# Kernel tuning notes

Hardware: AMD Instinct MI355X
Metric: run time of the kernel (lower is better)

## Reference

```python
import jax, jax.numpy as jnp
import numpy as np

B = 262144  # batch of joint configurations (original module processes one at a time)


def setup_inputs() -> dict:
    key = jax.random.key(0)
    k = jax.random.split(key, 7)
    joints = jax.random.normal(k[0], (B, 7), dtype=jnp.float32)
    # fk_params rows: (alpha, a, d, theta_offset) per joint
    fk_params = jax.random.normal(k[1], (7, 4), dtype=jnp.float32) * 0.5
    # nn.Linear(7,15), nn.Linear(15,15), nn.Linear(15,7): y = x @ W.T + b
    W1 = jax.random.normal(k[2], (15, 7), dtype=jnp.float32) * 0.3
    b1 = jax.random.normal(k[3], (15,), dtype=jnp.float32) * 0.1
    W2 = jax.random.normal(k[4], (15, 15), dtype=jnp.float32) * 0.3
    b2 = jax.random.normal(k[5], (15,), dtype=jnp.float32) * 0.1
    W3 = jax.random.normal(k[6], (7, 15), dtype=jnp.float32) * 0.3
    b3 = jnp.zeros((7,), dtype=jnp.float32)
    return {"joints": joints, "fk_params": fk_params,
            "W1": W1, "b1": b1, "W2": W2, "b2": b2, "W3": W3, "b3": b3}


def reference(joints, fk_params, W1, b1, W2, b2, W3, b3):
    # 7-15-15-7 tanh MLP correction
    h = jnp.tanh(joints @ W1.T + b1)
    h = jnp.tanh(h @ W2.T + b2)
    correction = jnp.tanh(h @ W3.T + b3)
    theta = joints + correction                         # [B,7]

    alpha = fk_params[:, 0]                             # [7]
    a = fk_params[:, 1]
    d = fk_params[:, 2]
    offset = fk_params[:, 3]

    th = theta + offset                                 # [B,7]
    ct, st = jnp.cos(th), jnp.sin(th)                   # [B,7]
    ca, sa = jnp.cos(alpha), jnp.sin(alpha)             # [7]
    z = jnp.zeros_like(ct)
    o = jnp.ones_like(ct)

    # DH transform per (batch, joint): [B,7,4,4]
    row0 = jnp.stack([ct,      -st,       z,       a * o      ], axis=-1)
    row1 = jnp.stack([st * ca,  ct * ca, -sa * o, -d * sa * o ], axis=-1)
    row2 = jnp.stack([st * sa,  ct * sa,  ca * o,  ca * d * o ], axis=-1)
    row3 = jnp.stack([z,        z,        z,       o          ], axis=-1)
    M = jnp.stack([row0, row1, row2, row3], axis=-2)    # [B,7,4,4]

    # serial chain multiply over the 7 joints (fixed, small loop)
    ee = M[:, 0]
    for j in range(1, 7):
        ee = ee @ M[:, j]

    # wrist_transform[:-1, -1] -> translation part
    return ee[:, :3, 3]                                 # [B,3]
```

## Files before the change

kernel.cpp:

```cpp
#include <hip/hip_runtime.h>
#include <math.h>

#define BLK 256

__device__ __forceinline__ float fast_tanh(float x) {
    x = fminf(9.0f, fmaxf(-9.0f, x));
    float e = __expf(2.0f * x);
    return fmaf(-2.0f, __builtin_amdgcn_rcpf(e + 1.0f), 1.0f);
}

__device__ __forceinline__ void fast_sincos(float x, float& s, float& c) {
    const float INV2PI = 0.15915494309189535f;
    float r = __builtin_amdgcn_fractf(x * INV2PI);
    s = __builtin_amdgcn_sinf(r);
    c = __builtin_amdgcn_cosf(r);
}

__global__ __launch_bounds__(BLK) void fk_fused_kernel(
    const float* __restrict__ joints,
    const float* __restrict__ fk_params,
    const float* __restrict__ W1, const float* __restrict__ b1,
    const float* __restrict__ W2, const float* __restrict__ b2,
    const float* __restrict__ W3, const float* __restrict__ b3,
    float* __restrict__ out,
    int B)
{
    __shared__ float sJ[BLK * 7];

    const int t = threadIdx.x;
    const int base = blockIdx.x * BLK;
    const bool full = (B - base) >= BLK;

    if (full) {
        const float4* gsrc = (const float4*)(joints + base * 7);
        float4* ldst = (float4*)sJ;
        ldst[t] = gsrc[t];
        { int i = t + BLK; if (i < (BLK * 7) / 4) ldst[i] = gsrc[i]; }
    } else {
        const int nval = (B - base) * 7;
        for (int i = t; i < nval; i += BLK) sJ[i] = joints[base * 7 + i];
    }
    __syncthreads();

    const int sample = base + t;
    const bool active = full || (sample < B);
    float r0[4], r1[4], r2[4];

    if (active) {
        float j[7];
        #pragma unroll
        for (int k = 0; k < 7; ++k) j[k] = sJ[t * 7 + k];

        float h1[15];
        #pragma unroll
        for (int i = 0; i < 15; ++i) {
            float s = b1[i];
            #pragma unroll
            for (int k = 0; k < 7; ++k) s = fmaf(j[k], W1[i * 7 + k], s);
            h1[i] = fast_tanh(s);
        }
        float h2[15];
        #pragma unroll
        for (int i = 0; i < 15; ++i) {
            float s = b2[i];
            #pragma unroll
            for (int k = 0; k < 15; ++k) s = fmaf(h1[k], W2[i * 15 + k], s);
            h2[i] = fast_tanh(s);
        }

        #pragma unroll
        for (int jj = 0; jj < 7; ++jj) {
            float s = b3[jj];
            #pragma unroll
            for (int k = 0; k < 15; ++k) s = fmaf(h2[k], W3[jj * 15 + k], s);
            float corr = fast_tanh(s);

            const float alpha = fk_params[jj * 4 + 0];
            const float a     = fk_params[jj * 4 + 1];
            const float d     = fk_params[jj * 4 + 2];
            const float off   = fk_params[jj * 4 + 3];

            float th = j[jj] + corr + off;
            float st, ct, sa, ca;
            fast_sincos(th, st, ct);
            fast_sincos(alpha, sa, ca);

            const float m10 = st * ca, m11 = ct * ca, m13 = -d * sa;
            const float m20 = st * sa, m21 = ct * sa, m23 = ca * d;
            if (jj == 0) {
                r0[0] = ct;  r0[1] = -st; r0[2] = 0.0f; r0[3] = a;
                r1[0] = m10; r1[1] = m11; r1[2] = -sa;  r1[3] = m13;
                r2[0] = m20; r2[1] = m21; r2[2] = ca;   r2[3] = m23;
            } else {
                #pragma unroll
                for (int i = 0; i < 1; ++i) { }
                float n0, n1, n2, n3;
                n0 = r0[0]*ct + r0[1]*m10 + r0[2]*m20;
                n1 = -r0[0]*st + r0[1]*m11 + r0[2]*m21;
                n2 =             r0[1]*-sa + r0[2]*ca;
                n3 = r0[0]*a  + r0[1]*m13 + r0[2]*m23 + r0[3];
                r0[0]=n0; r0[1]=n1; r0[2]=n2; r0[3]=n3;
                n0 = r1[0]*ct + r1[1]*m10 + r1[2]*m20;
                n1 = -r1[0]*st + r1[1]*m11 + r1[2]*m21;
                n2 =             r1[1]*-sa + r1[2]*ca;
                n3 = r1[0]*a  + r1[1]*m13 + r1[2]*m23 + r1[3];
                r1[0]=n0; r1[1]=n1; r1[2]=n2; r1[3]=n3;
                n0 = r2[0]*ct + r2[1]*m10 + r2[2]*m20;
                n1 = -r2[0]*st + r2[1]*m11 + r2[2]*m21;
                n2 =             r2[1]*-sa + r2[2]*ca;
                n3 = r2[0]*a  + r2[1]*m13 + r2[2]*m23 + r2[3];
                r2[0]=n0; r2[1]=n1; r2[2]=n2; r2[3]=n3;
            }
        }
    }

    __syncthreads();
    if (active) {
        sJ[t * 3 + 0] = r0[3];
        sJ[t * 3 + 1] = r1[3];
        sJ[t * 3 + 2] = r2[3];
    }
    __syncthreads();
    if (full) {
        float4* gdst = (float4*)(out + base * 3);
        const float4* lsrc = (const float4*)sJ;
        if (t < (BLK * 3) / 4) gdst[t] = lsrc[t];
    } else {
        const int onval = (B - base) * 3;
        for (int i = t; i < onval; i += BLK) out[base * 3 + i] = sJ[i];
    }
}

extern "C" void kernel_launch(void* const* d_in, const int* in_sizes, int n_in,
                              void* d_out, int out_size, void* d_ws, size_t ws_size,
                              hipStream_t stream) {
    const float* joints    = (const float*)d_in[0];
    const float* fk_params = (const float*)d_in[1];
    const float* W1 = (const float*)d_in[2];
    const float* b1 = (const float*)d_in[3];
    const float* W2 = (const float*)d_in[4];
    const float* b2 = (const float*)d_in[5];
    const float* W3 = (const float*)d_in[6];
    const float* b3 = (const float*)d_in[7];
    float* out = (float*)d_out;

    const int B = in_sizes[0] / 7;
    const int nblk = (B + BLK - 1) / BLK;
    fk_fused_kernel<<<nblk, BLK, 0, stream>>>(joints, fk_params, W1, b1, W2, b2,
                                              W3, b3, out, B);
}
```

Baseline: 79.62 us.

## Apply DH chain right-to-left as vector transform instead of matrix products

```diff
diff --git a/kernel.cpp b/kernel.cpp
--- a/kernel.cpp
+++ b/kernel.cpp
@@ -4,7 +4,6 @@
 #define BLK 256
 
 __device__ __forceinline__ float fast_tanh(float x) {
-    x = fminf(9.0f, fmaxf(-9.0f, x));
     float e = __expf(2.0f * x);
     return fmaf(-2.0f, __builtin_amdgcn_rcpf(e + 1.0f), 1.0f);
 }
@@ -44,7 +43,7 @@
 
     const int sample = base + t;
     const bool active = full || (sample < B);
-    float r0[4], r1[4], r2[4];
+    float v0 = 0.f, v1 = 0.f, v2 = 0.f;
 
     if (active) {
         float j[7];
@@ -68,57 +67,43 @@
             h2[i] = fast_tanh(s);
         }
 
+        float th[7];
         #pragma unroll
         for (int jj = 0; jj < 7; ++jj) {
             float s = b3[jj];
             #pragma unroll
             for (int k = 0; k < 15; ++k) s = fmaf(h2[k], W3[jj * 15 + k], s);
-            float corr = fast_tanh(s);
+            th[jj] = j[jj] + fast_tanh(s) + fk_params[jj * 4 + 3];
+        }
 
+        #pragma unroll
+        for (int jj = 6; jj >= 0; --jj) {
             const float alpha = fk_params[jj * 4 + 0];
             const float a     = fk_params[jj * 4 + 1];
             const float d     = fk_params[jj * 4 + 2];
-            const float off   = fk_params[jj * 4 + 3];
-
-            float th = j[jj] + corr + off;
             float st, ct, sa, ca;
-            fast_sincos(th, st, ct);
+            fast_sincos(th[jj], st, ct);
             fast_sincos(alpha, sa, ca);
-
-            const float m10 = st * ca, m11 = ct * ca, m13 = -d * sa;
-            const float m20 = st * sa, m21 = ct * sa, m23 = ca * d;
-            if (jj == 0) {
-                r0[0] = ct;  r0[1] = -st; r0[2] = 0.0f; r0[3] = a;
-                r1[0] = m10; r1[1] = m11; r1[2] = -sa;  r1[3] = m13;
-                r2[0] = m20; r2[1] = m21; r2[2] = ca;   r2[3] = m23;
+            if (jj == 6) {
+                v0 = a;
+                v1 = -d * sa;
+                v2 = d * ca;
             } else {
-                #pragma unroll
-                for (int i = 0; i < 1; ++i) { }
-                float n0, n1, n2, n3;
-                n0 = r0[0]*ct + r0[1]*m10 + r0[2]*m20;
-                n1 = -r0[0]*st + r0[1]*m11 + r0[2]*m21;
-                n2 =             r0[1]*-sa + r0[2]*ca;
-                n3 = r0[0]*a  + r0[1]*m13 + r0[2]*m23 + r0[3];
-                r0[0]=n0; r0[1]=n1; r0[2]=n2; r0[3]=n3;
-                n0 = r1[0]*ct + r1[1]*m10 + r1[2]*m20;
-                n1 = -r1[0]*st + r1[1]*m11 + r1[2]*m21;
-                n2 =             r1[1]*-sa + r1[2]*ca;
-                n3 = r1[0]*a  + r1[1]*m13 + r1[2]*m23 + r1[3];
-                r1[0]=n0; r1[1]=n1; r1[2]=n2; r1[3]=n3;
-                n0 = r2[0]*ct + r2[1]*m10 + r2[2]*m20;
-                n1 = -r2[0]*st + r2[1]*m11 + r2[2]*m21;
-                n2 =             r2[1]*-sa + r2[2]*ca;
-                n3 = r2[0]*a  + r2[1]*m13 + r2[2]*m23 + r2[3];
-                r2[0]=n0; r2[1]=n1; r2[2]=n2; r2[3]=n3;
+                const float t1 = fmaf(st, v0, ct * v1);
+                const float u  = v2 + d;
+                const float n0 = fmaf(ct, v0, fmaf(-st, v1, a));
+                v1 = fmaf(ca, t1, -sa * u);
+                v2 = fmaf(sa, t1, ca * u);
+                v0 = n0;
             }
         }
     }
 
     __syncthreads();
     if (active) {
-        sJ[t * 3 + 0] = r0[3];
-        sJ[t * 3 + 1] = r1[3];
-        sJ[t * 3 + 2] = r2[3];
+        sJ[t * 3 + 0] = v0;
+        sJ[t * 3 + 1] = v1;
+        sJ[t * 3 + 2] = v2;
     }
     __syncthreads();
     if (full) {
```

After: 79.28 us. About the same (-0.4%).
